# Kernel tuning notes

Hardware: AMD Instinct MI355X
Metric: run time of the kernel (lower is better)

Reference implementation:

```python
import jax, jax.numpy as jnp
import numpy as np

B, S, F, H = 2, 2048, 1024, 16
HD = F // H


def setup_inputs() -> dict:
    key = jax.random.key(0)
    ks = jax.random.split(key, 9)
    Q = jax.random.normal(ks[0], (B, S, F), dtype=jnp.float32)
    K = jax.random.normal(ks[1], (B, S, F), dtype=jnp.float32)
    V = jax.random.normal(ks[2], (B, S, F), dtype=jnp.float32)
    # additive pre-softmax causal mask: 0 on/below diagonal, -1e9 above
    causal = jnp.tril(jnp.ones((S, S), dtype=bool))
    mask_1 = jnp.where(causal, 0.0, -1e9).astype(jnp.float32)[None, None]
    # multiplicative post-softmax mask in [0,1)
    mask_2 = jax.random.uniform(ks[3], (1, 1, S, S), dtype=jnp.float32)
    scale = 1.0 / np.sqrt(F)
    W_q = jax.random.normal(ks[4], (F, F), dtype=jnp.float32) * scale
    W_k = jax.random.normal(ks[5], (F, F), dtype=jnp.float32) * scale
    W_v = jax.random.normal(ks[6], (F, F), dtype=jnp.float32) * scale
    W_o = jax.random.normal(ks[7], (F, F), dtype=jnp.float32) * scale
    return {"Q": Q, "K": K, "V": V, "mask_1": mask_1, "mask_2": mask_2,
            "W_q": W_q, "W_k": W_k, "W_v": W_v, "W_o": W_o}


def reference(Q, K, V, mask_1, mask_2, W_q, W_k, W_v, W_o):
    # Linear projections (no bias), split into heads: [B,S,F] -> [B,H,S,HD]
    def proj(x, W):
        return (x @ W.T).reshape(B, S, H, HD).transpose(0, 2, 1, 3)
    q, k, v = proj(Q, W_q), proj(K, W_k), proj(V, W_v)
    # scores [B,H,S,S], scaled by sqrt(head_size)
    scores = jnp.einsum('bhqd,bhkd->bhqk', q, k) / np.sqrt(HD)
    scores = scores + mask_1  # additive pre-softmax mask
    probs = jax.nn.softmax(scores, axis=-1) * mask_2  # multiplicative post-softmax mask
    out = jnp.einsum('bhqk,bhkd->bhqd', probs, v)
    out = out.transpose(0, 2, 1, 3).reshape(B, S, F)
    return out @ W_o.T
```

## Files before the change

### kernel.cpp

```cpp
#include <hip/hip_runtime.h>
#include <hip/hip_bf16.h>
#include <stdint.h>

typedef __bf16 bf16_t;
typedef __bf16 bf16x8 __attribute__((ext_vector_type(8)));
typedef __bf16 bf16x4v __attribute__((ext_vector_type(4)));
typedef float f32x4 __attribute__((ext_vector_type(4)));

#define GLDS16(g, l)                                                         \
  __builtin_amdgcn_global_load_lds(                                          \
      (const __attribute__((address_space(1))) void*)(g),                    \
      (__attribute__((address_space(3))) void*)(l), 16, 0, 0)

__device__ __forceinline__ f32x4 mfma16(bf16x8 a, bf16x8 b, f32x4 c) {
  return __builtin_amdgcn_mfma_f32_16x16x32_bf16(a, b, c, 0, 0, 0);
}

static constexpr int S = 2048, F = 1024, H = 16, HD = 64;

static constexpr size_t OFF_QB  = 0;
static constexpr size_t OFF_KB  = 4194304;
static constexpr size_t OFF_VB  = 8388608;
static constexpr size_t OFF_WQ  = 12582912;
static constexpr size_t OFF_WK  = 13631488;
static constexpr size_t OFF_WV  = 14680064;
static constexpr size_t OFF_WO  = 15728640;
static constexpr size_t OFF_QP  = 16777216;
static constexpr size_t OFF_KP  = 20971520;
static constexpr size_t OFF_VPT = 25165824;
static constexpr size_t OFF_M2  = 29360128;
static constexpr size_t OFF_ATT = 0;

__global__ void cvt_all(const float* __restrict__ s0, const float* __restrict__ s1,
                        const float* __restrict__ s2, const float* __restrict__ s3,
                        const float* __restrict__ w0, const float* __restrict__ w1,
                        const float* __restrict__ w2, const float* __restrict__ w3,
                        bf16_t* __restrict__ d0, bf16_t* __restrict__ d1,
                        bf16_t* __restrict__ d2, bf16_t* __restrict__ d3,
                        bf16_t* __restrict__ e0, bf16_t* __restrict__ e1,
                        bf16_t* __restrict__ e2, bf16_t* __restrict__ e3) {
  const float* s;
  bf16_t* d;
  size_t r;
  if (blockIdx.x < 8192) {
    int t = blockIdx.x * 256 + threadIdx.x;
    int a = t >> 19;
    r = (size_t)(t & 0x7FFFF) * 8;
    s = (a == 0) ? s0 : (a == 1) ? s1 : (a == 2) ? s2 : s3;
    d = (a == 0) ? d0 : (a == 1) ? d1 : (a == 2) ? d2 : d3;
  } else {
    int t = (blockIdx.x - 8192) * 256 + threadIdx.x;
    int a = t >> 17;
    r = (size_t)(t & 0x1FFFF) * 8;
    s = (a == 0) ? w0 : (a == 1) ? w1 : (a == 2) ? w2 : w3;
    d = (a == 0) ? e0 : (a == 1) ? e1 : (a == 2) ? e2 : e3;
  }
  const float4* sp = (const float4*)(s + r);
  float4 u = sp[0], v = sp[1];
  bf16x8 o;
  o[0] = (bf16_t)u.x; o[1] = (bf16_t)u.y; o[2] = (bf16_t)u.z; o[3] = (bf16_t)u.w;
  o[4] = (bf16_t)v.x; o[5] = (bf16_t)v.y; o[6] = (bf16_t)v.z; o[7] = (bf16_t)v.w;
  *(bf16x8*)(d + r) = o;
}

__device__ __forceinline__ void stage128x32(const bf16_t* __restrict__ g, int ld,
                                            bf16_t* lds, int wv, int ln) {
#pragma unroll
  for (int i = 0; i < 2; ++i) {
    int ch  = wv * 2 + i;
    int row = ch * 16 + (ln >> 2);
    int col = (ln & 3) * 8;
    GLDS16(g + (size_t)row * ld + col, lds + ch * 512);
  }
}

__global__ __launch_bounds__(256, 2) void proj_gemm(
    const bf16_t* __restrict__ Qb, const bf16_t* __restrict__ Kb, const bf16_t* __restrict__ Vb,
    const bf16_t* __restrict__ Wq, const bf16_t* __restrict__ Wk, const bf16_t* __restrict__ Wv,
    bf16_t* __restrict__ qp, bf16_t* __restrict__ kp, bf16_t* __restrict__ vpT) {
  __shared__ bf16_t As[2][128 * 32];
  __shared__ bf16_t Bs[2][128 * 32];
  const int z = blockIdx.z;
  const bf16_t* A = (z == 0) ? Qb : (z == 1) ? Kb : Vb;
  const bf16_t* W = (z == 0) ? Wq : (z == 1) ? Wk : Wv;
  const int m0 = blockIdx.x * 128, n0 = blockIdx.y * 128;
  const int tid = threadIdx.x, wv = tid >> 6, ln = tid & 63;
  const int wr = wv >> 1, wc = wv & 1, lr = ln & 15, lg = ln >> 4;
  f32x4 acc[4][4];
#pragma unroll
  for (int i = 0; i < 4; ++i)
#pragma unroll
    for (int j = 0; j < 4; ++j) acc[i][j] = (f32x4){0.f, 0.f, 0.f, 0.f};

  stage128x32(A + (size_t)m0 * F, F, As[0], wv, ln);
  stage128x32(W + (size_t)n0 * F, F, Bs[0], wv, ln);
  __syncthreads();

  for (int k0 = 0; k0 < F; k0 += 32) {
    const int cur = (k0 >> 5) & 1;
    if (k0 + 32 < F) {
      stage128x32(A + (size_t)m0 * F + k0 + 32, F, As[cur ^ 1], wv, ln);
      stage128x32(W + (size_t)n0 * F + k0 + 32, F, Bs[cur ^ 1], wv, ln);
    }
    bf16x8 af[4], bfr[4];
#pragma unroll
    for (int i = 0; i < 4; ++i)
      af[i] = *(const bf16x8*)&As[cur][(wr * 64 + i * 16 + lr) * 32 + lg * 8];
#pragma unroll
    for (int j = 0; j < 4; ++j)
      bfr[j] = *(const bf16x8*)&Bs[cur][(wc * 64 + j * 16 + lr) * 32 + lg * 8];
#pragma unroll
    for (int i = 0; i < 4; ++i)
#pragma unroll
      for (int j = 0; j < 4; ++j) acc[i][j] = mfma16(af[i], bfr[j], acc[i][j]);
    __syncthreads();
  }

  const int rbase = m0 + wr * 64, cbase = n0 + wc * 64;
  if (z < 2) {
    bf16_t* out = (z == 0) ? qp : kp;
    const float qscl = (z == 0) ? 0.18033688f : 1.0f;
#pragma unroll
    for (int i = 0; i < 4; ++i)
#pragma unroll
      for (int j = 0; j < 4; ++j) {
        int r0 = rbase + i * 16 + lg * 4;
        int c  = cbase + j * 16 + lr;
        int b = r0 >> 11, s = r0 & 2047, h = c >> 6, d = c & 63;
        size_t base = ((size_t)(b * H + h) * S + s) * HD + d;
#pragma unroll
        for (int reg = 0; reg < 4; ++reg)
          out[base + (size_t)reg * HD] = (bf16_t)(acc[i][j][reg] * qscl);
      }
  } else {
#pragma unroll
    for (int i = 0; i < 4; ++i)
#pragma unroll
      for (int j = 0; j < 4; ++j) {
        int r0 = rbase + i * 16 + lg * 4;
        int c  = cbase + j * 16 + lr;
        int b = r0 >> 11, s = r0 & 2047, h = c >> 6, d = c & 63;
        size_t base = ((size_t)(b * H + h) * HD + d) * S + s;
        bf16x4v pv;
#pragma unroll
        for (int reg = 0; reg < 4; ++reg) pv[reg] = (bf16_t)acc[i][j][reg];
        *(bf16x4v*)&vpT[base] = pv;
      }
  }
}

__global__ __launch_bounds__(256, 2) void out_gemm(
    const bf16_t* __restrict__ A, const bf16_t* __restrict__ W, float* __restrict__ out) {
  __shared__ bf16_t As[2][128 * 32];
  __shared__ bf16_t Bs[2][128 * 32];
  const int m0 = blockIdx.x * 128, n0 = blockIdx.y * 128;
  const int tid = threadIdx.x, wv = tid >> 6, ln = tid & 63;
  const int wr = wv >> 1, wc = wv & 1, lr = ln & 15, lg = ln >> 4;
  f32x4 acc[4][4];
#pragma unroll
  for (int i = 0; i < 4; ++i)
#pragma unroll
    for (int j = 0; j < 4; ++j) acc[i][j] = (f32x4){0.f, 0.f, 0.f, 0.f};

  stage128x32(A + (size_t)m0 * F, F, As[0], wv, ln);
  stage128x32(W + (size_t)n0 * F, F, Bs[0], wv, ln);
  __syncthreads();

  for (int k0 = 0; k0 < F; k0 += 32) {
    const int cur = (k0 >> 5) & 1;
    if (k0 + 32 < F) {
      stage128x32(A + (size_t)m0 * F + k0 + 32, F, As[cur ^ 1], wv, ln);
      stage128x32(W + (size_t)n0 * F + k0 + 32, F, Bs[cur ^ 1], wv, ln);
    }
    bf16x8 af[4], bfr[4];
#pragma unroll
    for (int i = 0; i < 4; ++i)
      af[i] = *(const bf16x8*)&As[cur][(wr * 64 + i * 16 + lr) * 32 + lg * 8];
#pragma unroll
    for (int j = 0; j < 4; ++j)
      bfr[j] = *(const bf16x8*)&Bs[cur][(wc * 64 + j * 16 + lr) * 32 + lg * 8];
#pragma unroll
    for (int i = 0; i < 4; ++i)
#pragma unroll
      for (int j = 0; j < 4; ++j) acc[i][j] = mfma16(af[i], bfr[j], acc[i][j]);
    __syncthreads();
  }
#pragma unroll
  for (int i = 0; i < 4; ++i)
#pragma unroll
    for (int j = 0; j < 4; ++j) {
      int r0 = m0 + wr * 64 + i * 16 + lg * 4;
      int c  = n0 + wc * 64 + j * 16 + lr;
#pragma unroll
      for (int reg = 0; reg < 4; ++reg)
        out[(size_t)(r0 + reg) * F + c] = acc[i][j][reg];
    }
}

__global__ __launch_bounds__(256, 4) void flash(
    const bf16_t* __restrict__ qp, const bf16_t* __restrict__ kp,
    const bf16_t* __restrict__ vpT, const bf16_t* __restrict__ m2b,
    bf16_t* __restrict__ attn) {
  __shared__ bf16_t Ks[2][64 * 64];
  __shared__ bf16_t Vs[2][64 * 64];
  __shared__ bf16_t Pl[4][16 * 64];
  const int qt = (int)gridDim.x - 1 - (int)blockIdx.x;
  const int bh = blockIdx.y;
  const int tid = threadIdx.x, wv = tid >> 6, ln = tid & 63;
  const int lr = ln & 15, lg = ln >> 4;
  const bf16_t* qb = qp + (size_t)bh * S * HD;
  const bf16_t* kb = kp + (size_t)bh * S * HD;
  const bf16_t* vb = vpT + (size_t)bh * HD * S;
  const int q0w = qt * 64 + wv * 16;
  const int qg  = q0w + lr;

  bf16x8 bq[2];
#pragma unroll
  for (int h2 = 0; h2 < 2; ++h2)
    bq[h2] = *(const bf16x8*)&qb[(size_t)qg * HD + h2 * 32 + lg * 8];

  float ls = 0.f;
  f32x4 accv[4];
#pragma unroll
  for (int n = 0; n < 4; ++n) accv[n] = (f32x4){0.f, 0.f, 0.f, 0.f};

  const int srow0 = ln >> 3, scc0 = ln & 7;
  const int pxor = lr & 7;

#pragma unroll
  for (int i = 0; i < 2; ++i) {
    int ch = wv * 2 + i;
    int row = ch * 8 + srow0;
    int scc = scc0 ^ (row & 7);
    GLDS16(kb + (size_t)row * HD + scc * 8, Ks[0] + ch * 512);
    GLDS16(vb + (size_t)row * S + scc * 8, Vs[0] + ch * 512);
  }
  __syncthreads();

  for (int kt = 0; kt <= qt; ++kt) {
    const int k0 = kt * 64;
    const int cur = kt & 1;

    bf16x4v m2v[4];
#pragma unroll
    for (int c = 0; c < 4; ++c)
      m2v[c] = *(const bf16x4v*)&m2b[(size_t)qg * S + k0 + c * 16 + lg * 4];

    if (kt < qt) {
      const int kn = k0 + 64;
#pragma unroll
      for (int i = 0; i < 2; ++i) {
        int ch = wv * 2 + i;
        int row = ch * 8 + srow0;
        int scc = scc0 ^ (row & 7);
        GLDS16(kb + (size_t)(kn + row) * HD + scc * 8, Ks[cur ^ 1] + ch * 512);
        GLDS16(vb + (size_t)row * S + kn + scc * 8, Vs[cur ^ 1] + ch * 512);
      }
    }

    f32x4 st[4];
    __builtin_amdgcn_s_setprio(1);
#pragma unroll
    for (int c = 0; c < 4; ++c) {
      int kr = c * 16 + lr;
      int sw = kr & 7;
      bf16x8 ak0 = *(const bf16x8*)&Ks[cur][kr * 64 + ((lg ^ sw) * 8)];
      bf16x8 ak1 = *(const bf16x8*)&Ks[cur][kr * 64 + (((4 + lg) ^ sw) * 8)];
      f32x4 t = (f32x4){0.f, 0.f, 0.f, 0.f};
      t = mfma16(ak0, bq[0], t);
      t = mfma16(ak1, bq[1], t);
      st[c] = t;
    }
    __builtin_amdgcn_s_setprio(0);
    if (kt == qt) {
#pragma unroll
      for (int c = 0; c < 4; ++c)
#pragma unroll
        for (int r = 0; r < 4; ++r) {
          int kgl = k0 + c * 16 + lg * 4 + r;
          if (kgl > qg) st[c][r] = -1e30f;
        }
    }
#pragma unroll
    for (int c = 0; c < 4; ++c) {
      bf16x4v pw;
      float p0 = exp2f(st[c][0]), p1 = exp2f(st[c][1]);
      float p2 = exp2f(st[c][2]), p3 = exp2f(st[c][3]);
      ls += (p0 + p1) + (p2 + p3);
      pw[0] = (bf16_t)(p0 * (float)m2v[c][0]);
      pw[1] = (bf16_t)(p1 * (float)m2v[c][1]);
      pw[2] = (bf16_t)(p2 * (float)m2v[c][2]);
      pw[3] = (bf16_t)(p3 * (float)m2v[c][3]);
      int chunk = (2 * c + (lg >> 1)) ^ pxor;
      *(bf16x4v*)&Pl[wv][lr * 64 + chunk * 8 + (lg & 1) * 4] = pw;
    }
    __builtin_amdgcn_s_setprio(1);
#pragma unroll
    for (int kc = 0; kc < 2; ++kc) {
      int pchunk = (4 * kc + lg) ^ pxor;
      bf16x8 pb = *(const bf16x8*)&Pl[wv][lr * 64 + pchunk * 8];
#pragma unroll
      for (int n = 0; n < 4; ++n) {
        int dr = n * 16 + lr;
        int sw = dr & 7;
        bf16x8 av = *(const bf16x8*)&Vs[cur][dr * 64 + (((kc * 4 + lg) ^ sw) * 8)];
        accv[n] = mfma16(av, pb, accv[n]);
      }
    }
    __builtin_amdgcn_s_setprio(0);
    __syncthreads();
  }

  ls += __shfl_xor(ls, 16, 64);
  ls += __shfl_xor(ls, 32, 64);
  const int b = bh >> 4, h = bh & 15;
  const float inv = 1.0f / ls;
#pragma unroll
  for (int n = 0; n < 4; ++n) {
    bf16x4v ov;
#pragma unroll
    for (int r = 0; r < 4; ++r) ov[r] = (bf16_t)(accv[n][r] * inv);
    *(bf16x4v*)&attn[(size_t)(b * S + qg) * F + h * HD + n * 16 + lg * 4] = ov;
  }
}

extern "C" void kernel_launch(void* const* d_in, const int* in_sizes, int n_in,
                              void* d_out, int out_size, void* d_ws, size_t ws_size,
                              hipStream_t stream) {
  (void)in_sizes; (void)n_in; (void)out_size; (void)ws_size;
  const float* Q  = (const float*)d_in[0];
  const float* K  = (const float*)d_in[1];
  const float* V  = (const float*)d_in[2];
  const float* M2 = (const float*)d_in[4];
  const float* Wq = (const float*)d_in[5];
  const float* Wk = (const float*)d_in[6];
  const float* Wv = (const float*)d_in[7];
  const float* Wo = (const float*)d_in[8];
  bf16_t* ws = (bf16_t*)d_ws;

  bf16_t *Qb = ws + OFF_QB, *Kb = ws + OFF_KB, *Vb = ws + OFF_VB;
  bf16_t *WqB = ws + OFF_WQ, *WkB = ws + OFF_WK, *WvB = ws + OFF_WV, *WoB = ws + OFF_WO;
  bf16_t *qpB = ws + OFF_QP, *kpB = ws + OFF_KP, *vpT = ws + OFF_VPT;
  bf16_t *m2b = ws + OFF_M2, *att = ws + OFF_ATT;

  cvt_all<<<10240, 256, 0, stream>>>(Q, K, V, M2, Wq, Wk, Wv, Wo,
                                     Qb, Kb, Vb, m2b, WqB, WkB, WvB, WoB);
  proj_gemm<<<dim3(32, 8, 3), 256, 0, stream>>>(Qb, Kb, Vb, WqB, WkB, WvB, qpB, kpB, vpT);
  flash<<<dim3(32, 32), 256, 0, stream>>>(qpB, kpB, vpT, m2b, att);
  out_gemm<<<dim3(32, 8), 256, 0, stream>>>(att, WoB, (float*)d_out);
}
```

Measured before the change: 158.5 us.

## Split long causal query tiles across two KV ranges and merge in a normalize kernel

The flash kernel's work is rebalanced. Query tiles in the upper half, which have the most causal KV tiles, are split into two blocks that each process half of the KV range. Partial unnormalized outputs and row sums go to workspace buffers that reuse the no-longer-needed input staging areas. A new norm_cvt kernel sums the partials, normalizes them and writes the attention layout. The split relies on the softmax having no running max, so partials add directly. The aim is to reduce the causal tail imbalance and raise occupancy, at the cost of an extra kernel launch and an extra round trip of the partial buffers through memory.

```diff
diff --git a/kernel.cpp b/kernel.cpp
--- a/kernel.cpp
+++ b/kernel.cpp
@@ -200,12 +200,24 @@
 __global__ __launch_bounds__(256, 4) void flash(
     const bf16_t* __restrict__ qp, const bf16_t* __restrict__ kp,
     const bf16_t* __restrict__ vpT, const bf16_t* __restrict__ m2b,
-    bf16_t* __restrict__ attn) {
+    bf16_t* __restrict__ PA, bf16_t* __restrict__ PB,
+    float* __restrict__ lA, float* __restrict__ lB) {
   __shared__ bf16_t Ks[2][64 * 64];
   __shared__ bf16_t Vs[2][64 * 64];
   __shared__ bf16_t Pl[4][16 * 64];
-  const int qt = (int)gridDim.x - 1 - (int)blockIdx.x;
-  const int bh = blockIdx.y;
+  const int ur = blockIdx.x >> 5, bh = blockIdx.x & 31;
+  const int grp = ur / 3, rem = ur % 3;
+  int qt, kvlo, kvhi;
+  if (rem == 2) { qt = 15 - grp; kvlo = 0; kvhi = qt; }
+  else {
+    qt = 31 - grp;
+    int half = (qt + 2) >> 1;
+    if (rem == 0) { kvlo = 0; kvhi = half - 1; }
+    else          { kvlo = half; kvhi = qt; }
+  }
+  bf16_t* __restrict__ PO = (rem == 1) ? PB : PA;
+  float*  __restrict__ LO = (rem == 1) ? lB : lA;
+
   const int tid = threadIdx.x, wv = tid >> 6, ln = tid & 63;
   const int lr = ln & 15, lg = ln >> 4;
   const bf16_t* qb = qp + (size_t)bh * S * HD;
@@ -232,21 +244,21 @@
     int ch = wv * 2 + i;
     int row = ch * 8 + srow0;
     int scc = scc0 ^ (row & 7);
-    GLDS16(kb + (size_t)row * HD + scc * 8, Ks[0] + ch * 512);
-    GLDS16(vb + (size_t)row * S + scc * 8, Vs[0] + ch * 512);
+    GLDS16(kb + (size_t)(kvlo * 64 + row) * HD + scc * 8, Ks[0] + ch * 512);
+    GLDS16(vb + (size_t)row * S + kvlo * 64 + scc * 8, Vs[0] + ch * 512);
   }
   __syncthreads();
 
-  for (int kt = 0; kt <= qt; ++kt) {
+  for (int kt = kvlo; kt <= kvhi; ++kt) {
     const int k0 = kt * 64;
-    const int cur = kt & 1;
+    const int cur = (kt - kvlo) & 1;
 
     bf16x4v m2v[4];
 #pragma unroll
     for (int c = 0; c < 4; ++c)
       m2v[c] = *(const bf16x4v*)&m2b[(size_t)qg * S + k0 + c * 16 + lg * 4];
 
-    if (kt < qt) {
+    if (kt < kvhi) {
       const int kn = k0 + 64;
 #pragma unroll
       for (int i = 0; i < 2; ++i) {
@@ -313,15 +325,49 @@
 
   ls += __shfl_xor(ls, 16, 64);
   ls += __shfl_xor(ls, 32, 64);
-  const int b = bh >> 4, h = bh & 15;
-  const float inv = 1.0f / ls;
+  if (lg == 0) LO[bh * S + qg] = ls;
 #pragma unroll
   for (int n = 0; n < 4; ++n) {
     bf16x4v ov;
 #pragma unroll
-    for (int r = 0; r < 4; ++r) ov[r] = (bf16_t)(accv[n][r] * inv);
-    *(bf16x4v*)&attn[(size_t)(b * S + qg) * F + h * HD + n * 16 + lg * 4] = ov;
-  }
+    for (int r = 0; r < 4; ++r) ov[r] = (bf16_t)accv[n][r];
+    *(bf16x4v*)&PO[((size_t)bh * S + qg) * HD + n * 16 + lg * 4] = ov;
+  }
+}
+
+__global__ void norm_cvt(const bf16_t* __restrict__ PA, const bf16_t* __restrict__ PB,
+                         const float* __restrict__ lA, const float* __restrict__ lB,
+                         bf16_t* __restrict__ att) {
+  int t = blockIdx.x * 256 + threadIdx.x;
+  int bh = t >> 13;
+  int rm = t & 8191;
+  int s  = rm >> 2;
+  int d0 = (rm & 3) * 16;
+  size_t pbase = ((size_t)bh * S + s) * HD + d0;
+  bf16x8 a0 = *(const bf16x8*)&PA[pbase];
+  bf16x8 a1 = *(const bf16x8*)&PA[pbase + 8];
+  float l = lA[bh * S + s];
+  float o[16];
+#pragma unroll
+  for (int i = 0; i < 8; ++i) { o[i] = (float)a0[i]; o[8 + i] = (float)a1[i]; }
+  if (s >= 1024) {
+    bf16x8 b0 = *(const bf16x8*)&PB[pbase];
+    bf16x8 b1 = *(const bf16x8*)&PB[pbase + 8];
+    l += lB[bh * S + s];
+#pragma unroll
+    for (int i = 0; i < 8; ++i) { o[i] += (float)b0[i]; o[8 + i] += (float)b1[i]; }
+  }
+  float inv = 1.0f / l;
+  int b = bh >> 4, h = bh & 15;
+  bf16x8 w0, w1;
+#pragma unroll
+  for (int i = 0; i < 8; ++i) {
+    w0[i] = (bf16_t)(o[i] * inv);
+    w1[i] = (bf16_t)(o[8 + i] * inv);
+  }
+  size_t obase = ((size_t)(b * S + s)) * F + h * HD + d0;
+  *(bf16x8*)&att[obase] = w0;
+  *(bf16x8*)&att[obase + 8] = w1;
 }
 
 extern "C" void kernel_launch(void* const* d_in, const int* in_sizes, int n_in,
@@ -342,10 +388,13 @@
   bf16_t *WqB = ws + OFF_WQ, *WkB = ws + OFF_WK, *WvB = ws + OFF_WV, *WoB = ws + OFF_WO;
   bf16_t *qpB = ws + OFF_QP, *kpB = ws + OFF_KP, *vpT = ws + OFF_VPT;
   bf16_t *m2b = ws + OFF_M2, *att = ws + OFF_ATT;
+  bf16_t *PA = ws + OFF_KB, *PB = ws + OFF_VB;
+  float  *lA = (float*)(ws + OFF_WQ), *lB = (float*)(ws + OFF_WK);
 
   cvt_all<<<10240, 256, 0, stream>>>(Q, K, V, M2, Wq, Wk, Wv, Wo,
                                      Qb, Kb, Vb, m2b, WqB, WkB, WvB, WoB);
   proj_gemm<<<dim3(32, 8, 3), 256, 0, stream>>>(Qb, Kb, Vb, WqB, WkB, WvB, qpB, kpB, vpT);
-  flash<<<dim3(32, 32), 256, 0, stream>>>(qpB, kpB, vpT, m2b, att);
+  flash<<<dim3(1536), 256, 0, stream>>>(qpB, kpB, vpT, m2b, PA, PB, lA, lB);
+  norm_cvt<<<1024, 256, 0, stream>>>(PA, PB, lA, lB, att);
   out_gemm<<<dim3(32, 8), 256, 0, stream>>>(att, WoB, (float*)d_out);
 }
```

Result: faster. 137.3 us (median of 2 runs) (-13.3%).
